# Kernel tuning notes

Hardware: AMD Instinct MI355X
Metric: run time of the kernel (lower is better)

The kernel has to match this reference:

```python
import math
import jax, jax.numpy as jnp
import numpy as np

N_HEADS = 8
FACTOR = 1


def setup_inputs() -> dict:
    key = jax.random.key(0)
    ks = jax.random.split(key, 8)
    B, L, D = 8, 2048, 512
    scale = 0.05
    return {
        "queries": jax.random.normal(ks[0], (B, L, D), jnp.float32),
        "keys": jax.random.normal(ks[1], (B, L, D), jnp.float32),
        "values": jax.random.normal(ks[2], (B, L, D), jnp.float32),
        "Wq": jax.random.normal(ks[3], (D, D), jnp.float32) * scale,
        "bq": jnp.zeros((D,), jnp.float32),
        "Wk": jax.random.normal(ks[4], (D, D), jnp.float32) * scale,
        "bk": jnp.zeros((D,), jnp.float32),
        "Wv": jax.random.normal(ks[5], (D, D), jnp.float32) * scale,
        "bv": jnp.zeros((D,), jnp.float32),
        "Wo": jax.random.normal(ks[6], (D, D), jnp.float32) * scale,
        "bo": jnp.zeros((D,), jnp.float32),
    }


def _autocorrelation(q, k, v):
    # q,k,v: [B, L, H, E]; L == S assumed (as built in setup_inputs)
    B, L, H, E = q.shape
    qp = jnp.transpose(q, (0, 2, 3, 1))  # [B,H,E,L]
    kp = jnp.transpose(k, (0, 2, 3, 1))
    vp = jnp.transpose(v, (0, 2, 3, 1))
    q_fft = jnp.fft.rfft(qp, axis=-1)
    k_fft = jnp.fft.rfft(kp, axis=-1)
    corr = jnp.fft.irfft(q_fft * jnp.conj(k_fft), n=L, axis=-1)  # [B,H,E,L]

    # training-path time-delay aggregation
    top_k = int(FACTOR * math.log(L))  # static python int
    mean_value = corr.mean(axis=(1, 2))  # [B, L]
    _, index = jax.lax.top_k(mean_value.mean(axis=0), top_k)  # [K] global delays
    weights = mean_value[:, index]  # [B, K]
    tmp_corr = jax.nn.softmax(weights, axis=-1)  # [B, K]
    # roll(v, -d) along last axis == gather at (t + d) mod L
    idx = (jnp.arange(L)[None, :] + index[:, None]) % L  # [K, L]
    patterns = vp[..., idx]  # [B,H,E,K,L]
    delays_agg = jnp.einsum('bhekl,bk->bhel', patterns, tmp_corr)  # [B,H,E,L]
    return jnp.transpose(delays_agg, (0, 3, 1, 2))  # [B,L,H,E]


def reference(queries, keys, values, Wq, bq, Wk, bk, Wv, bv, Wo, bo):
    B, L, Dm = queries.shape
    H = N_HEADS
    q = (queries @ Wq + bq).reshape(B, L, H, -1)
    k = (keys @ Wk + bk).reshape(B, L, H, -1)
    v = (values @ Wv + bv).reshape(B, L, H, -1)
    out = _autocorrelation(q, k, v).reshape(B, L, -1)
    return out @ Wo + bo
```

## Files before the change

### kernel.cpp

```cpp
#include <hip/hip_runtime.h>
#include <stdint.h>

#define BATCH 8
#define L_SEQ 2048
#define D_MODEL 512
#define TOPK 7
#define BM 128
#define BN 128
#define BK 32
#define LK 40
#define LT 136

typedef _Float16 f16x8 __attribute__((ext_vector_type(8)));
typedef __attribute__((ext_vector_type(4))) float f32x4;
typedef unsigned short u16;
typedef unsigned int u32;

__device__ __forceinline__ u16 f2h(float f) {
    union { _Float16 h; u16 u; } v; v.h = (_Float16)f; return v.u;
}

__device__ __forceinline__ void load_lds16(const u16* g, u16* l) {
    __builtin_amdgcn_global_load_lds(
        (const __attribute__((address_space(1))) u32*)(g),
        (__attribute__((address_space(3))) u32*)(l), 16, 0, 0);
}

__global__ __launch_bounds__(256) void gemm_qkv(
    const float* __restrict__ Xq, const float* __restrict__ Xk, const float* __restrict__ Xv,
    const u16* __restrict__ Wqt, const u16* __restrict__ Wkt, const u16* __restrict__ Wvt,
    const float* __restrict__ bq, const float* __restrict__ bk, const float* __restrict__ bv,
    u16* __restrict__ QT, u16* __restrict__ KT, u16* __restrict__ Vout)
{
    __shared__ __align__(16) u16 lA[BM * LK];
    __shared__ __align__(16) u16 lB[BN * LK];
    __shared__ __align__(16) u16 lT[64 * LT];

    const int tid = threadIdx.x;
    const int bn = blockIdx.x, bm = blockIdx.y, z = blockIdx.z;
    const int lane = tid & 63, wave = tid >> 6;
    const int wm = wave >> 1, wn = wave & 1;
    const int l15 = lane & 15, quad = lane >> 4;

    const float* A  = (z == 0) ? Xq  : (z == 1) ? Xk  : Xv;
    const u16*   Bt = (z == 0) ? Wqt : (z == 1) ? Wkt : Wvt;
    const float* bias = (z == 0) ? bq : (z == 1) ? bk : bv;

    f32x4 acc[4][4] = {};

    for (int k0 = 0; k0 < D_MODEL; k0 += BK) {
        #pragma unroll
        for (int j = 0; j < 4; ++j) {
            int idx = tid + j * 256;
            int row = idx >> 3, c4 = (idx & 7) * 4;
            float4 va = *(const float4*)(A + (long)(bm * BM + row) * D_MODEL + k0 + c4);
            ushort4 pa;
            pa.x = f2h(va.x); pa.y = f2h(va.y); pa.z = f2h(va.z); pa.w = f2h(va.w);
            *(ushort4*)&lA[row * LK + c4] = pa;
        }
        #pragma unroll
        for (int j = 0; j < 2; ++j) {
            int idx = tid + j * 256;
            int row = idx >> 2, c8 = (idx & 3) * 8;
            *(uint4*)&lB[row * LK + c8] =
                *(const uint4*)(Bt + (long)(bn * BN + row) * D_MODEL + k0 + c8);
        }
        __syncthreads();

        f16x8 fa[4], fb[4];
        #pragma unroll
        for (int i = 0; i < 4; ++i)
            fa[i] = *(const f16x8*)&lA[(wm * 64 + i * 16 + l15) * LK + quad * 8];
        #pragma unroll
        for (int j = 0; j < 4; ++j)
            fb[j] = *(const f16x8*)&lB[(wn * 64 + j * 16 + l15) * LK + quad * 8];
        #pragma unroll
        for (int i = 0; i < 4; ++i)
            #pragma unroll
            for (int j = 0; j < 4; ++j)
                acc[i][j] = __builtin_amdgcn_mfma_f32_16x16x32_f16(fa[i], fb[j], acc[i][j], 0, 0, 0);
        __syncthreads();
    }

    if (z < 2) {
        u16* out = (z == 0) ? QT : KT;
        const int t0 = (bm * BM) & (L_SEQ - 1);
        const int bb = (bm * BM) >> 11;
        #pragma unroll
        for (int h = 0; h < 2; ++h) {
            __syncthreads();
            if (wn == h) {
                #pragma unroll
                for (int j = 0; j < 4; ++j) {
                    int dloc = j * 16 + l15;
                    float bvv = bias[bn * BN + h * 64 + dloc];
                    #pragma unroll
                    for (int i = 0; i < 4; ++i) {
                        int trow = wm * 64 + i * 16 + quad * 4;
                        #pragma unroll
                        for (int r = 0; r < 4; ++r)
                            lT[dloc * LT + trow + r] = f2h(acc[i][j][r] + bvv);
                    }
                }
            }
            __syncthreads();
            int dloc = tid >> 2, q4 = tid & 3;
            long base = ((long)(bb * D_MODEL + bn * BN + h * 64 + dloc)) * L_SEQ + t0;
            #pragma unroll
            for (int s = 0; s < 4; ++s) {
                int c = q4 * 4 + s;
                *(uint4*)(out + base + c * 8) = *(const uint4*)&lT[dloc * LT + c * 8];
            }
        }
    } else {
        #pragma unroll
        for (int i = 0; i < 4; ++i) {
            int row = bm * BM + wm * 64 + i * 16 + quad * 4;
            #pragma unroll
            for (int j = 0; j < 4; ++j) {
                int col = bn * BN + wn * 64 + j * 16 + l15;
                float bvv = bias[col];
                #pragma unroll
                for (int r = 0; r < 4; ++r)
                    Vout[(long)(row + r) * D_MODEL + col] = f2h(acc[i][j][r] + bvv);
            }
        }
    }
}

__global__ __launch_bounds__(256) void gemm_out_fused(
    const u16* __restrict__ V, const u16* __restrict__ Bt,
    const int* __restrict__ selIdx, const float* __restrict__ selW,
    const float* __restrict__ bias, float* __restrict__ Cp)
{
    __shared__ __align__(16) u16 lA[BM * LK];
    __shared__ __align__(16) u16 lB[BN * BK];
    __shared__ int   si[TOPK];
    __shared__ float sw[BATCH][TOPK];

    const int tid = threadIdx.x;
    const int bn = blockIdx.x, bm = blockIdx.y;
    const int lane = tid & 63, wave = tid >> 6;
    const int wm = wave >> 1, wn = wave & 1;
    const int l15 = lane & 15, quad = lane >> 4;

    if (tid < TOPK) si[tid] = selIdx[tid];
    if (tid < BATCH * TOPK) sw[tid / TOPK][tid % TOPK] = selW[tid];

    const int s0 = wave * 64 + lane, s1 = s0 + 256;
    const int r0 = s0 >> 2, c0 = (s0 & 3) ^ ((r0 >> 1) & 3);
    const int r1 = s1 >> 2, c1 = (s1 & 3) ^ ((r1 >> 1) & 3);
    const u16* gB0 = Bt + (long)(bn * BN + r0) * D_MODEL + c0 * 8;
    const u16* gB1 = Bt + (long)(bn * BN + r1) * D_MODEL + c1 * 8;
    u16* lB0 = &lB[wave * 512]; u16* lB1 = &lB[2048 + wave * 512];

    __syncthreads();

    f32x4 acc[4][4] = {};

    for (int k0 = 0; k0 < D_MODEL; k0 += BK) {
        load_lds16(gB0, lB0); load_lds16(gB1, lB1);
        gB0 += BK; gB1 += BK;
        #pragma unroll
        for (int j = 0; j < 2; ++j) {
            int idx = tid + j * 256;
            int row = idx >> 2, c8 = (idx & 3) * 8;
            int gr = bm * BM + row;
            int b = gr >> 11, l = gr & (L_SEQ - 1);
            float a[8] = {0,0,0,0,0,0,0,0};
            #pragma unroll
            for (int k = 0; k < TOPK; ++k) {
                int src = (l + si[k]) & (L_SEQ - 1);
                union { uint4 u; _Float16 h[8]; } x;
                x.u = *(const uint4*)(V + ((long)b * L_SEQ + src) * D_MODEL + k0 + c8);
                float w = sw[b][k];
                #pragma unroll
                for (int q = 0; q < 8; ++q) a[q] += w * (float)x.h[q];
            }
            union { uint4 u; u16 s[8]; } o;
            #pragma unroll
            for (int q = 0; q < 8; ++q) o.s[q] = f2h(a[q]);
            *(uint4*)&lA[row * LK + c8] = o.u;
        }
        __syncthreads();

        f16x8 fa[4], fb[4];
        #pragma unroll
        for (int i = 0; i < 4; ++i)
            fa[i] = *(const f16x8*)&lA[(wm * 64 + i * 16 + l15) * LK + quad * 8];
        #pragma unroll
        for (int j = 0; j < 4; ++j) {
            int n = wn * 64 + j * 16 + l15;
            int cs = quad ^ ((n >> 1) & 3);
            fb[j] = *(const f16x8*)&lB[n * 32 + cs * 8];
        }
        #pragma unroll
        for (int i = 0; i < 4; ++i)
            #pragma unroll
            for (int j = 0; j < 4; ++j)
                acc[i][j] = __builtin_amdgcn_mfma_f32_16x16x32_f16(fa[i], fb[j], acc[i][j], 0, 0, 0);
        __syncthreads();
    }

    #pragma unroll
    for (int i = 0; i < 4; ++i) {
        int row = bm * BM + wm * 64 + i * 16 + quad * 4;
        #pragma unroll
        for (int j = 0; j < 4; ++j) {
            int col = bn * BN + wn * 64 + j * 16 + l15;
            float bvv = bias[col];
            #pragma unroll
            for (int r = 0; r < 4; ++r)
                Cp[(long)(row + r) * D_MODEL + col] = acc[i][j][r] + bvv;
        }
    }
}

__device__ __forceinline__ void fft2048_lds(
    float* Zr, float* Zi, const float* Twr, const float* Twi, int tid)
{
    #pragma unroll
    for (int s = 0; s < 10; s += 2) {
        #pragma unroll
        for (int u = 0; u < 2; ++u) {
            int idx = tid + u * 256;
            int d1 = 1 << s;
            int pos = idx & (d1 - 1);
            int i0 = ((idx >> s) << (s + 2)) + pos;
            float w1r = Twr[pos << (10 - s)], w1i = Twi[pos << (10 - s)];
            float w2r = Twr[pos << (9 - s)],  w2i = Twi[pos << (9 - s)];
            int p2 = pos + d1;
            float w3r = Twr[p2 << (9 - s)],   w3i = Twi[p2 << (9 - s)];
            float ar = Zr[i0],          ai = Zi[i0];
            float br = Zr[i0 + d1],     bi = Zi[i0 + d1];
            float cr = Zr[i0 + 2 * d1], ci = Zi[i0 + 2 * d1];
            float dr = Zr[i0 + 3 * d1], di = Zi[i0 + 3 * d1];
            float t1r = br * w1r - bi * w1i, t1i = br * w1i + bi * w1r;
            float Ar = ar + t1r, Ai = ai + t1i, Br = ar - t1r, Bi = ai - t1i;
            float t2r = dr * w1r - di * w1i, t2i = dr * w1i + di * w1r;
            float Cr = cr + t2r, Ci = ci + t2i, Dr = cr - t2r, Di = ci - t2i;
            float u1r = Cr * w2r - Ci * w2i, u1i = Cr * w2i + Ci * w2r;
            float u2r = Dr * w3r - Di * w3i, u2i = Dr * w3i + Di * w3r;
            Zr[i0]          = Ar + u1r; Zi[i0]          = Ai + u1i;
            Zr[i0 + 2 * d1] = Ar - u1r; Zi[i0 + 2 * d1] = Ai - u1i;
            Zr[i0 + d1]     = Br + u2r; Zi[i0 + d1]     = Bi + u2i;
            Zr[i0 + 3 * d1] = Br - u2r; Zi[i0 + 3 * d1] = Bi - u2i;
        }
        __syncthreads();
    }
    #pragma unroll
    for (int j = 0; j < 4; ++j) {
        int idx = tid + j * 256;
        float wr = Twr[idx], wi = Twi[idx];
        float ar = Zr[idx], ai = Zi[idx];
        float br = Zr[idx + 1024], bi = Zi[idx + 1024];
        float tr = br * wr - bi * wi, ti = br * wi + bi * wr;
        Zr[idx] = ar + tr; Zi[idx] = ai + ti;
        Zr[idx + 1024] = ar - tr; Zi[idx + 1024] = ai - ti;
    }
    __syncthreads();
}

__global__ __launch_bounds__(256) void fft_corr_fwd(
    const u16* __restrict__ QT, const u16* __restrict__ KT, float* __restrict__ S)
{
    __shared__ float Zr[2048], Zi[2048];
    __shared__ float Sr[2048], Si[2048];
    __shared__ float Twr[1024], Twi[1024];
    const int tid = threadIdx.x;
    const int b = blockIdx.x >> 6, dg = blockIdx.x & 63;

    #pragma unroll
    for (int j = 0; j < 4; ++j) {
        int i = tid + j * 256;
        float ang = -6.28318530717958647692f * (float)i * (1.0f / 2048.0f);
        float sn, cs; __sincosf(ang, &sn, &cs);
        Twr[i] = cs; Twi[i] = sn;
    }
    #pragma unroll
    for (int j = 0; j < 8; ++j) { Sr[tid + j * 256] = 0.f; Si[tid + j * 256] = 0.f; }

    for (int g = 0; g < 8; ++g) {
        int d = dg * 8 + g;
        const u16* qrow = QT + ((long)b * D_MODEL + d) * L_SEQ;
        const u16* krow = KT + ((long)b * D_MODEL + d) * L_SEQ;
        __syncthreads();
        union { uint4 u; _Float16 h[8]; } xq, xk;
        xq.u = *(const uint4*)(qrow + tid * 8);
        xk.u = *(const uint4*)(krow + tid * 8);
        #pragma unroll
        for (int j = 0; j < 8; ++j) {
            int t = tid * 8 + j;
            int tr = (int)(__brev((unsigned)t) >> 21);
            Zr[tr] = (float)xq.h[j];
            Zi[tr] = (float)xk.h[j];
        }
        __syncthreads();
        fft2048_lds(Zr, Zi, Twr, Twi, tid);
        #pragma unroll
        for (int j = 0; j < 8; ++j) {
            int f = tid + j * 256;
            int fm = (2048 - f) & 2047;
            float Xr = Zr[f], Xi = Zi[f], Xmr = Zr[fm], Xmi = Zi[fm];
            float qr = 0.5f * (Xr + Xmr), qi = 0.5f * (Xi - Xmi);
            float dr = Xr - Xmr,          di = Xi + Xmi;
            float kr = 0.5f * di,         ki = -0.5f * dr;
            Sr[f] += qr * kr + qi * ki;
            Si[f] += qi * kr - qr * ki;
        }
    }
    __syncthreads();
    #pragma unroll
    for (int j = 0; j < 8; ++j) {
        int f = tid + j * 256;
        atomicAdd(&S[((long)b * 2048 + f) * 2 + 0], Sr[f]);
        atomicAdd(&S[((long)b * 2048 + f) * 2 + 1], Si[f]);
    }
}

__global__ __launch_bounds__(256) void fft_corr_inv(
    const float* __restrict__ S, float* __restrict__ raw)
{
    __shared__ float Zr[2048], Zi[2048];
    __shared__ float Twr[1024], Twi[1024];
    const int tid = threadIdx.x;
    const int b = blockIdx.x;

    #pragma unroll
    for (int j = 0; j < 4; ++j) {
        int i = tid + j * 256;
        float ang = 6.28318530717958647692f * (float)i * (1.0f / 2048.0f);
        float sn, cs; __sincosf(ang, &sn, &cs);
        Twr[i] = cs; Twi[i] = sn;
    }
    #pragma unroll
    for (int j = 0; j < 8; ++j) {
        int f = tid + j * 256;
        int fr = (int)(__brev((unsigned)f) >> 21);
        Zr[fr] = S[((long)b * 2048 + f) * 2 + 0];
        Zi[fr] = S[((long)b * 2048 + f) * 2 + 1];
    }
    __syncthreads();
    fft2048_lds(Zr, Zi, Twr, Twi, tid);
    #pragma unroll
    for (int j = 0; j < 8; ++j) {
        int t = tid + j * 256;
        raw[(long)b * 2048 + t] = Zr[t] * (1.0f / 2048.0f);
    }
}

__global__ __launch_bounds__(256) void transposeW4(
    const float* __restrict__ Wq, const float* __restrict__ Wk,
    const float* __restrict__ Wv, const float* __restrict__ Wo, u16* __restrict__ dstBase)
{
    __shared__ float t[32][33];
    const int z = blockIdx.z;
    const float* src = (z == 0) ? Wq : (z == 1) ? Wk : (z == 2) ? Wv : Wo;
    u16* dst = dstBase + (long)z * D_MODEL * D_MODEL;
    int tx = threadIdx.x & 31, ty = threadIdx.x >> 5;
    int c0 = blockIdx.x * 32, r0 = blockIdx.y * 32;
    #pragma unroll
    for (int r = ty; r < 32; r += 8)
        t[r][tx] = src[(long)(r0 + r) * D_MODEL + c0 + tx];
    __syncthreads();
    #pragma unroll
    for (int r = ty; r < 32; r += 8)
        dst[(long)(c0 + r) * D_MODEL + r0 + tx] = f2h(t[tx][r]);
}

__global__ __launch_bounds__(256) void select_topk(
    const float* __restrict__ raw, int* __restrict__ selIdx, float* __restrict__ selW)
{
    __shared__ float g[L_SEQ];
    __shared__ float rv[256];
    __shared__ int   ri[256];
    __shared__ int   sidx[TOPK];
    __shared__ float wbuf[BATCH][TOPK];
    int tid = threadIdx.x;
    for (int t = tid; t < L_SEQ; t += 256) {
        float s = 0.0f;
        #pragma unroll
        for (int b = 0; b < BATCH; ++b) s += raw[b * L_SEQ + t];
        g[t] = s;
    }
    __syncthreads();
    for (int it = 0; it < TOPK; ++it) {
        float best = -1e30f; int bi = 0x7fffffff;
        for (int t = tid; t < L_SEQ; t += 256) {
            float v = g[t];
            if (v > best || (v == best && t < bi)) { best = v; bi = t; }
        }
        rv[tid] = best; ri[tid] = bi;
        __syncthreads();
        for (int s = 128; s > 0; s >>= 1) {
            if (tid < s) {
                float v2 = rv[tid + s]; int i2 = ri[tid + s];
                if (v2 > rv[tid] || (v2 == rv[tid] && i2 < ri[tid])) { rv[tid] = v2; ri[tid] = i2; }
            }
            __syncthreads();
        }
        if (tid == 0) { sidx[it] = ri[0]; g[ri[0]] = -1e30f; }
        __syncthreads();
    }
    if (tid < BATCH * TOPK) {
        int b = tid / TOPK, k = tid % TOPK;
        wbuf[b][k] = raw[b * L_SEQ + sidx[k]] * (1.0f / 512.0f);
    }
    __syncthreads();
    if (tid < BATCH) {
        float mx = -1e30f;
        #pragma unroll
        for (int k = 0; k < TOPK; ++k) mx = fmaxf(mx, wbuf[tid][k]);
        float e[TOPK]; float sum = 0.0f;
        #pragma unroll
        for (int k = 0; k < TOPK; ++k) { e[k] = expf(wbuf[tid][k] - mx); sum += e[k]; }
        #pragma unroll
        for (int k = 0; k < TOPK; ++k) selW[tid * TOPK + k] = e[k] / sum;
    }
    if (tid < TOPK) selIdx[tid] = sidx[tid];
}

extern "C" void kernel_launch(void* const* d_in, const int* in_sizes, int n_in,
                              void* d_out, int out_size, void* d_ws, size_t ws_size,
                              hipStream_t stream)
{
    (void)in_sizes; (void)n_in; (void)out_size; (void)ws_size;
    const float* Xq = (const float*)d_in[0];
    const float* Xk = (const float*)d_in[1];
    const float* Xv = (const float*)d_in[2];
    const float* Wq = (const float*)d_in[3];
    const float* bq = (const float*)d_in[4];
    const float* Wk = (const float*)d_in[5];
    const float* bk = (const float*)d_in[6];
    const float* Wv = (const float*)d_in[7];
    const float* bv = (const float*)d_in[8];
    const float* Wo = (const float*)d_in[9];
    const float* bo = (const float*)d_in[10];

    char* ws = (char*)d_ws;
    const long SLABH = (long)BATCH * L_SEQ * D_MODEL * sizeof(u16);
    u16* QT   = (u16*)(ws);
    u16* KT   = (u16*)(ws + SLABH);
    u16* Vf   = (u16*)(ws + 2 * SLABH);
    const long WSZ = (long)D_MODEL * D_MODEL;
    u16* Wt   = (u16*)(ws + 3 * SLABH);
    u16* Wqt = Wt + 0 * WSZ; u16* Wkt = Wt + 1 * WSZ;
    u16* Wvt = Wt + 2 * WSZ; u16* Wot = Wt + 3 * WSZ;
    float* S   = (float*)(ws + 3 * SLABH + 4 * WSZ * sizeof(u16));
    float* raw = S + (long)BATCH * L_SEQ * 2;
    int*   sIdx = (int*)(raw + (long)BATCH * L_SEQ);
    float* sW   = (float*)(sIdx + 8);

    dim3 tb(256);
    transposeW4<<<dim3(16, 16, 4), tb, 0, stream>>>(Wq, Wk, Wv, Wo, Wt);
    hipMemsetAsync(S, 0, (long)BATCH * L_SEQ * 2 * sizeof(float), stream);

    dim3 gP(D_MODEL / BN, (BATCH * L_SEQ) / BM, 3);
    gemm_qkv<<<gP, tb, 0, stream>>>(Xq, Xk, Xv, Wqt, Wkt, Wvt, bq, bk, bv, QT, KT, Vf);

    fft_corr_fwd<<<dim3(512), tb, 0, stream>>>(QT, KT, S);
    fft_corr_inv<<<dim3(BATCH), tb, 0, stream>>>(S, raw);
    select_topk<<<1, tb, 0, stream>>>(raw, sIdx, sW);

    dim3 gO(D_MODEL / BN, (BATCH * L_SEQ) / BM, 1);
    gemm_out_fused<<<gO, tb, 0, stream>>>(Vf, Wot, sIdx, sW, bo, (float*)d_out);
}
```

Baseline: 344.5 us.

## Remap GEMM blocks across XCDs, load weights via async LDS, and alias shared memory

Both GEMM kernels now use a 1D grid with a remapping so that consecutive logical tiles land on the same XCD (hw&7 chunking), which improves L2 locality for shared A/B tiles. In gemm_qkv the weight tile is loaded with global_load_lds directly into a swizzled LDS layout instead of through registers. The A, B and transpose-staging buffers are aliased into one shared array, which shrinks LDS use and may raise occupancy. Aliasing lT over lA/lB depends on the epilogue syncs to avoid a race, and the XOR swizzle must match the read pattern.

```diff
diff --git a/kernel.cpp b/kernel.cpp
--- a/kernel.cpp
+++ b/kernel.cpp
@@ -32,12 +32,16 @@
     const float* __restrict__ bq, const float* __restrict__ bk, const float* __restrict__ bv,
     u16* __restrict__ QT, u16* __restrict__ KT, u16* __restrict__ Vout)
 {
-    __shared__ __align__(16) u16 lA[BM * LK];
-    __shared__ __align__(16) u16 lB[BN * LK];
-    __shared__ __align__(16) u16 lT[64 * LT];
+    __shared__ __align__(16) u16 smem[BM * LK + BN * BK];
+    u16* lA = smem;
+    u16* lB = smem + BM * LK;
+    u16* lT = smem;
 
     const int tid = threadIdx.x;
-    const int bn = blockIdx.x, bm = blockIdx.y, z = blockIdx.z;
+    const int hw = blockIdx.x;
+    const int lg = (hw & 7) * 192 + (hw >> 3);
+    const int bn = lg & 3, bm = (lg >> 2) & 127, z = lg >> 9;
+
     const int lane = tid & 63, wave = tid >> 6;
     const int wm = wave >> 1, wn = wave & 1;
     const int l15 = lane & 15, quad = lane >> 4;
@@ -46,9 +50,18 @@
     const u16*   Bt = (z == 0) ? Wqt : (z == 1) ? Wkt : Wvt;
     const float* bias = (z == 0) ? bq : (z == 1) ? bk : bv;
 
+    const int s0 = wave * 64 + lane, s1 = s0 + 256;
+    const int r0 = s0 >> 2, c0 = (s0 & 3) ^ ((r0 >> 1) & 3);
+    const int r1 = s1 >> 2, c1 = (s1 & 3) ^ ((r1 >> 1) & 3);
+    const u16* gB0 = Bt + (long)(bn * BN + r0) * D_MODEL + c0 * 8;
+    const u16* gB1 = Bt + (long)(bn * BN + r1) * D_MODEL + c1 * 8;
+    u16* lB0 = &lB[wave * 512]; u16* lB1 = &lB[2048 + wave * 512];
+
     f32x4 acc[4][4] = {};
 
     for (int k0 = 0; k0 < D_MODEL; k0 += BK) {
+        load_lds16(gB0, lB0); load_lds16(gB1, lB1);
+        gB0 += BK; gB1 += BK;
         #pragma unroll
         for (int j = 0; j < 4; ++j) {
             int idx = tid + j * 256;
@@ -58,13 +71,6 @@
             pa.x = f2h(va.x); pa.y = f2h(va.y); pa.z = f2h(va.z); pa.w = f2h(va.w);
             *(ushort4*)&lA[row * LK + c4] = pa;
         }
-        #pragma unroll
-        for (int j = 0; j < 2; ++j) {
-            int idx = tid + j * 256;
-            int row = idx >> 2, c8 = (idx & 3) * 8;
-            *(uint4*)&lB[row * LK + c8] =
-                *(const uint4*)(Bt + (long)(bn * BN + row) * D_MODEL + k0 + c8);
-        }
         __syncthreads();
 
         f16x8 fa[4], fb[4];
@@ -72,8 +78,11 @@
         for (int i = 0; i < 4; ++i)
             fa[i] = *(const f16x8*)&lA[(wm * 64 + i * 16 + l15) * LK + quad * 8];
         #pragma unroll
-        for (int j = 0; j < 4; ++j)
-            fb[j] = *(const f16x8*)&lB[(wn * 64 + j * 16 + l15) * LK + quad * 8];
+        for (int j = 0; j < 4; ++j) {
+            int n = wn * 64 + j * 16 + l15;
+            int cs = quad ^ ((n >> 1) & 3);
+            fb[j] = *(const f16x8*)&lB[n * 32 + cs * 8];
+        }
         #pragma unroll
         for (int i = 0; i < 4; ++i)
             #pragma unroll
@@ -139,7 +148,10 @@
     __shared__ float sw[BATCH][TOPK];
 
     const int tid = threadIdx.x;
-    const int bn = blockIdx.x, bm = blockIdx.y;
+    const int hw = blockIdx.x;
+    const int lg = (hw & 7) * 64 + (hw >> 3);
+    const int bn = lg & 3, bm = lg >> 2;
+
     const int lane = tid & 63, wave = tid >> 6;
     const int wm = wave >> 1, wn = wave & 1;
     const int l15 = lane & 15, quad = lane >> 4;
@@ -455,13 +467,11 @@
     transposeW4<<<dim3(16, 16, 4), tb, 0, stream>>>(Wq, Wk, Wv, Wo, Wt);
     hipMemsetAsync(S, 0, (long)BATCH * L_SEQ * 2 * sizeof(float), stream);
 
-    dim3 gP(D_MODEL / BN, (BATCH * L_SEQ) / BM, 3);
-    gemm_qkv<<<gP, tb, 0, stream>>>(Xq, Xk, Xv, Wqt, Wkt, Wvt, bq, bk, bv, QT, KT, Vf);
+    gemm_qkv<<<dim3(1536), tb, 0, stream>>>(Xq, Xk, Xv, Wqt, Wkt, Wvt, bq, bk, bv, QT, KT, Vf);
 
     fft_corr_fwd<<<dim3(512), tb, 0, stream>>>(QT, KT, S);
     fft_corr_inv<<<dim3(BATCH), tb, 0, stream>>>(S, raw);
     select_topk<<<1, tb, 0, stream>>>(raw, sIdx, sW);
 
-    dim3 gO(D_MODEL / BN, (BATCH * L_SEQ) / BM, 1);
-    gemm_out_fused<<<gO, tb, 0, stream>>>(Vf, Wot, sIdx, sW, bo, (float*)d_out);
-}
+    gemm_out_fused<<<dim3(512), tb, 0, stream>>>(Vf, Wot, sIdx, sW, bo, (float*)d_out);
+}
```

Result: faster. 333.7 us (-3.1%).
